# Kernel optimization log

Hardware: AMD Instinct MI355X
Metric: run time of the kernel (lower is better)

The kernel has to match this reference:

```python
import jax, jax.numpy as jnp
import numpy as np

N_NODES = 100000
N_EDGES = 1600000
N_ETYPES = 3
IN_FEATS = 128
HEADS = 4
OUT_FEATS = 16
EDGE_FEATS = 64
NEG_SLOPE = 0.2


def setup_inputs() -> dict:
    key = jax.random.key(0)
    ks = jax.random.split(key, 10)
    return {
        "x": jax.random.normal(ks[0], (N_NODES, IN_FEATS), jnp.float32),
        "W": jax.random.normal(ks[1], (IN_FEATS, HEADS * OUT_FEATS), jnp.float32) * 0.05,
        "W_e": jax.random.normal(ks[2], (EDGE_FEATS, HEADS * EDGE_FEATS), jnp.float32) * 0.05,
        "attn_l": jax.random.normal(ks[3], (HEADS, OUT_FEATS), jnp.float32) * 0.1,
        "attn_r": jax.random.normal(ks[4], (HEADS, OUT_FEATS), jnp.float32) * 0.1,
        "attn_e": jax.random.normal(ks[5], (HEADS, EDGE_FEATS), jnp.float32) * 0.1,
        "edge_emb": jax.random.normal(ks[6], (N_ETYPES, EDGE_FEATS), jnp.float32),
        "src": jax.random.randint(ks[7], (N_EDGES,), 0, N_NODES, jnp.int32),
        "dst": jax.random.randint(ks[8], (N_EDGES,), 0, N_NODES, jnp.int32),
        "etype": jax.random.randint(ks[9], (N_EDGES,), 0, N_ETYPES, jnp.int32),
    }


def reference(x, W, W_e, attn_l, attn_r, attn_e, edge_emb, src, dst, etype):
    N = x.shape[0]
    H, D = attn_l.shape
    # node projection: [N, H, D]
    feat = (x @ W).reshape(N, H, D)
    # per-node attention halves: [N, H]
    el = jnp.einsum("nhd,hd->nh", feat, attn_l)
    er = jnp.einsum("nhd,hd->nh", feat, attn_r)
    # per-etype edge term: [T, H]
    e_feat = (edge_emb @ W_e).reshape(edge_emb.shape[0], H, -1)
    ee = jnp.einsum("the,he->th", e_feat, attn_e)
    # per-edge pre-softmax score: [E, H]
    s = el[src] + er[dst] + ee[etype]
    s = jnp.where(s > 0, s, NEG_SLOPE * s)  # leaky_relu
    # edge softmax over incoming edges of each dst node (homogeneous graph)
    m = jax.ops.segment_max(s, dst, num_segments=N)
    e = jnp.exp(s - m[dst])
    z = jax.ops.segment_sum(e, dst, num_segments=N)
    a = e / z[dst]  # [E, H]
    # u_mul_e + sum aggregation: [N, H, D]
    msg = feat[src] * a[:, :, None]
    rst = jax.ops.segment_sum(msg, dst, num_segments=N)
    return rst, a
```

## Files before the change

### kernel.cpp

```cpp
#include <hip/hip_runtime.h>
#include <hip/hip_bf16.h>

#define N_NODES   100000
#define N_EDGES   1600000
#define N_ETYPES  3
#define IN_FEATS  128
#define HEADS     4
#define OUT_FEATS 16
#define EDGE_FEATS 64
#define HD        64
#define NEG_SLOPE 0.2f
#define MAXD_LDS  128

#define NBUCK     800
#define NPB       125
#define PBLK      400
#define EPB       4000
#define BCAP      2560

typedef short s16x8 __attribute__((ext_vector_type(8)));
typedef float f32x4 __attribute__((ext_vector_type(4)));

__device__ __forceinline__ short f2bs(float f) {
    __hip_bfloat16 h = __float2bfloat16(f);
    return *reinterpret_cast<short*>(&h);
}

__global__ __launch_bounds__(256) void wt_prep_kernel(
    const float* __restrict__ W, short* __restrict__ WTb)
{
    const int t = blockIdx.x * 256 + threadIdx.x;
    const int k = t >> 6, n = t & 63;
    WTb[n * IN_FEATS + k] = f2bs(W[t]);
}

#define XS_STRIDE 136
__global__ __launch_bounds__(256) void feat_el_er_kernel(
    const float* __restrict__ x,
    const short* __restrict__ WTb,
    const float* __restrict__ attn_l,
    const float* __restrict__ attn_r,
    __hip_bfloat16* __restrict__ featb,
    float* __restrict__ el,
    float* __restrict__ er)
{
    __shared__ short Xs[16 * XS_STRIDE];
    __shared__ short Ws[64 * XS_STRIDE];

    const int t = threadIdx.x;
    const int row0 = blockIdx.x * 16;
    {
        const int r = t >> 4, k0 = (t & 15) * 8;
        const float4* xg = (const float4*)(x + (size_t)(row0 + r) * IN_FEATS + k0);
        const float4 v0 = xg[0], v1 = xg[1];
        s16x8 p;
        p[0] = f2bs(v0.x); p[1] = f2bs(v0.y); p[2] = f2bs(v0.z); p[3] = f2bs(v0.w);
        p[4] = f2bs(v1.x); p[5] = f2bs(v1.y); p[6] = f2bs(v1.z); p[7] = f2bs(v1.w);
        *(s16x8*)&Xs[r * XS_STRIDE + k0] = p;
    }
    {
#pragma unroll
        for (int j = 0; j < 4; ++j) {
            const int u = t + 256 * j;
            const int r = u >> 4, c = (u & 15) * 8;
            *(s16x8*)&Ws[r * XS_STRIDE + c] = *(const s16x8*)(WTb + r * IN_FEATS + c);
        }
    }
    __syncthreads();

    const int w    = t >> 6;
    const int lane = t & 63;
    const int m    = lane & 15;
    const int q    = lane >> 4;

    f32x4 acc = {0.f, 0.f, 0.f, 0.f};
#pragma unroll
    for (int kb = 0; kb < 4; ++kb) {
        const s16x8 af = *(const s16x8*)&Xs[m * XS_STRIDE + kb * 32 + q * 8];
        const s16x8 bf = *(const s16x8*)&Ws[(w * 16 + m) * XS_STRIDE + kb * 32 + q * 8];
        acc = __builtin_amdgcn_mfma_f32_16x16x32_bf16(af, bf, acc, 0, 0, 0);
    }

    const float al = attn_l[w * OUT_FEATS + m];
    const float ar = attn_r[w * OUT_FEATS + m];
#pragma unroll
    for (int r = 0; r < 4; ++r) {
        const int row = row0 + q * 4 + r;
        featb[(size_t)row * HD + w * 16 + m] = __float2bfloat16(acc[r]);
        float cl = acc[r] * al;
        float cr = acc[r] * ar;
#pragma unroll
        for (int msk = 1; msk < 16; msk <<= 1) {
            cl += __shfl_xor(cl, msk, 64);
            cr += __shfl_xor(cr, msk, 64);
        }
        if (m == 0) {
            el[row * HEADS + w] = cl;
            er[row * HEADS + w] = cr;
        }
    }
}

__global__ __launch_bounds__(64) void ee_kernel(
    const float* __restrict__ edge_emb,
    const float* __restrict__ W_e,
    const float* __restrict__ attn_e,
    float* __restrict__ ee)
{
    const int b  = blockIdx.x;
    const int ty = b >> 2;
    const int h  = b & 3;
    const int e  = threadIdx.x;

    float ef = 0.f;
#pragma unroll
    for (int k = 0; k < EDGE_FEATS; ++k)
        ef += edge_emb[ty * EDGE_FEATS + k] *
              W_e[k * (HEADS * EDGE_FEATS) + h * EDGE_FEATS + e];
    float v = ef * attn_e[h * EDGE_FEATS + e];
#pragma unroll
    for (int m = 1; m < 64; m <<= 1) v += __shfl_xor(v, m, 64);
    if (e == 0) ee[ty * HEADS + h] = v;
}

__global__ __launch_bounds__(256) void bucket_hist_kernel(
    const int* __restrict__ dst, int* __restrict__ bhist)
{
    __shared__ int h[NBUCK];
    const int t = threadIdx.x, b = blockIdx.x;
    for (int j = t; j < NBUCK; j += 256) h[j] = 0;
    __syncthreads();
    const int e0 = b * EPB;
    for (int i = t; i < EPB; i += 256)
        atomicAdd(&h[dst[e0 + i] / NPB], 1);
    __syncthreads();
    for (int j = t; j < NBUCK; j += 256) bhist[b * NBUCK + j] = h[j];
}

__global__ __launch_bounds__(256) void bucket_scan1_kernel(
    int* __restrict__ bhist, int* __restrict__ btot)
{
    __shared__ int sh[PBLK];
    const int t = threadIdx.x, j = blockIdx.x;
    const int j0 = t, j1 = t + 256;
    int o0 = 0, o1 = 0;
    if (j0 < PBLK) { o0 = bhist[j0 * NBUCK + j]; sh[j0] = o0; }
    if (j1 < PBLK) { o1 = bhist[j1 * NBUCK + j]; sh[j1] = o1; }
    __syncthreads();
    for (int off = 1; off < PBLK; off <<= 1) {
        int v0 = (j0 >= off && j0 < PBLK) ? sh[j0 - off] : 0;
        int v1 = (j1 >= off && j1 < PBLK) ? sh[j1 - off] : 0;
        __syncthreads();
        if (j0 < PBLK) sh[j0] += v0;
        if (j1 < PBLK) sh[j1] += v1;
        __syncthreads();
    }
    if (j0 < PBLK) bhist[j0 * NBUCK + j] = sh[j0] - o0;
    if (j1 < PBLK) bhist[j1 * NBUCK + j] = sh[j1] - o1;
    if (t == 255) btot[j] = sh[PBLK - 1];
}

__global__ __launch_bounds__(1024) void bucket_scan2_kernel(
    const int* __restrict__ btot, int* __restrict__ bbase)
{
    __shared__ int sh[NBUCK];
    const int t = threadIdx.x;
    int o = 0;
    if (t < NBUCK) { o = btot[t]; sh[t] = o; }
    __syncthreads();
    for (int off = 1; off < NBUCK; off <<= 1) {
        int v = (t >= off && t < NBUCK) ? sh[t - off] : 0;
        __syncthreads();
        if (t < NBUCK) sh[t] += v;
        __syncthreads();
    }
    if (t < NBUCK) bbase[t] = sh[t] - o;
    if (t == NBUCK - 1) bbase[NBUCK] = sh[t];
}

__global__ __launch_bounds__(256) void bucket_scatter_kernel(
    const int* __restrict__ src, const int* __restrict__ dst,
    const int* __restrict__ etype,
    const int* __restrict__ bhist, const int* __restrict__ bbase,
    int2* __restrict__ sc_bucket)
{
    __shared__ int cnt[NBUCK];
    const int t = threadIdx.x, b = blockIdx.x;
    for (int j = t; j < NBUCK; j += 256)
        cnt[j] = bbase[j] + bhist[b * NBUCK + j];
    __syncthreads();
    const int e0 = b * EPB;
    for (int i = t; i < EPB; i += 256) {
        const int e  = e0 + i;
        const int dn = dst[e];
        const int bu = dn / NPB;
        const int ld = dn - bu * NPB;
        const int slot = atomicAdd(&cnt[bu], 1);
        sc_bucket[slot] = make_int2(src[e], e | (etype[e] << 21) | (ld << 23));
    }
}

__global__ __launch_bounds__(256) void bucket_csr_kernel(
    const int2* __restrict__ sc_bucket, const int* __restrict__ bbase,
    int* __restrict__ ptr, int2* __restrict__ sc_csr)
{
    __shared__ int2 sbuf[BCAP];
    __shared__ int sdeg[128];
    __shared__ int scur[128];
    const int t = threadIdx.x, b = blockIdx.x;
    const int lo = bbase[b];
    const int count = bbase[b + 1] - lo;
    const bool staged = (count <= BCAP);

    if (t < 128) sdeg[t] = 0;
    __syncthreads();
    if (staged) {
        for (int i = t; i < count; i += 256) {
            const int2 v = sc_bucket[lo + i];
            sbuf[i] = v;
            atomicAdd(&sdeg[(v.y >> 23) & 0x7F], 1);
        }
    } else {
        for (int i = t; i < count; i += 256)
            atomicAdd(&sdeg[(sc_bucket[lo + i].y >> 23) & 0x7F], 1);
    }
    __syncthreads();
    const int orig = (t < 128) ? sdeg[t] : 0;
    for (int off = 1; off < 128; off <<= 1) {
        const int v = (t < 128 && t >= off) ? sdeg[t - off] : 0;
        __syncthreads();
        if (t < 128) sdeg[t] += v;
        __syncthreads();
    }
    if (t < 128) {
        const int excl = sdeg[t] - orig;
        if (t < NPB) ptr[b * NPB + t] = lo + excl;
        scur[t] = lo + excl;
    }
    if (b == 0 && t == 0) ptr[N_NODES] = N_EDGES;
    __syncthreads();
    if (staged) {
        for (int i = t; i < count; i += 256) {
            const int2 v = sbuf[i];
            const int ld = (v.y >> 23) & 0x7F;
            const int slot = atomicAdd(&scur[ld], 1);
            sc_csr[slot] = make_int2(v.x, (v.y & 0x1FFFFF) | (((v.y >> 21) & 3) << 24));
        }
    } else {
        for (int i = t; i < count; i += 256) {
            const int2 v = sc_bucket[lo + i];
            const int ld = (v.y >> 23) & 0x7F;
            const int slot = atomicAdd(&scur[ld], 1);
            sc_csr[slot] = make_int2(v.x, (v.y & 0x1FFFFF) | (((v.y >> 21) & 3) << 24));
        }
    }
}

__global__ __launch_bounds__(256) void agg_kernel(
    const int2* __restrict__ sc_csr, const int* __restrict__ ptr,
    const float* __restrict__ el, const float* __restrict__ er,
    const float* __restrict__ ee, const __hip_bfloat16* __restrict__ featb,
    float* __restrict__ rst, float* __restrict__ a_out)
{
    __shared__ float w_lds[4][MAXD_LDS * HEADS];
    const int wid  = threadIdx.x >> 6;
    const int lane = threadIdx.x & 63;
    const int n    = blockIdx.x * 4 + wid;

    const int p0  = ptr[n];
    const int deg = ptr[n + 1] - p0;
    float* wl = w_lds[wid];
    const ushort* fb = (const ushort*)featb;

    if (deg <= MAXD_LDS) {
        const int half  = lane >> 5;
        const int cpair = lane & 31;
        const int hB    = cpair >> 3;
        const bool accL = (cpair & 7) == 0;
        const float er_n = er[n * HEADS + hB];
        const float g0 = ee[hB], g1 = ee[HEADS + hB], g2 = ee[2 * HEADS + hB];

        float zacc = 0.f, rx = 0.f, ry = 0.f;
        int i = 0;
        for (; i + 4 <= deg; i += 4) {
            const int2 sc0 = sc_csr[p0 + i + half];
            const int2 sc1 = sc_csr[p0 + i + 2 + half];
            const uint f0 = *(const uint*)(fb + ((size_t)sc0.x << 6) + (cpair << 1));
            const uint f1 = *(const uint*)(fb + ((size_t)sc1.x << 6) + (cpair << 1));
            const float el0 = el[sc0.x * HEADS + hB];
            const float el1 = el[sc1.x * HEADS + hB];
            const int ty0 = sc0.y >> 24, ty1 = sc1.y >> 24;
            float s0 = el0 + er_n + ((ty0 == 0) ? g0 : ((ty0 == 1) ? g1 : g2));
            float s1 = el1 + er_n + ((ty1 == 0) ? g0 : ((ty1 == 1) ? g1 : g2));
            s0 = s0 > 0.f ? s0 : NEG_SLOPE * s0;
            s1 = s1 > 0.f ? s1 : NEG_SLOPE * s1;
            const float w0 = __expf(s0), w1 = __expf(s1);
            if (accL) {
                zacc += w0 + w1;
                wl[(i + half) * HEADS + hB]     = w0;
                wl[(i + 2 + half) * HEADS + hB] = w1;
            }
            rx += __uint_as_float(f0 << 16) * w0 + __uint_as_float(f1 << 16) * w1;
            ry += __uint_as_float(f0 & 0xFFFF0000u) * w0 + __uint_as_float(f1 & 0xFFFF0000u) * w1;
        }
        if (i + 2 <= deg) {
            const int2 sc0 = sc_csr[p0 + i + half];
            const uint f0 = *(const uint*)(fb + ((size_t)sc0.x << 6) + (cpair << 1));
            const float el0 = el[sc0.x * HEADS + hB];
            const int ty0 = sc0.y >> 24;
            float s0 = el0 + er_n + ((ty0 == 0) ? g0 : ((ty0 == 1) ? g1 : g2));
            s0 = s0 > 0.f ? s0 : NEG_SLOPE * s0;
            const float w0 = __expf(s0);
            if (accL) {
                zacc += w0;
                wl[(i + half) * HEADS + hB] = w0;
            }
            rx += __uint_as_float(f0 << 16) * w0;
            ry += __uint_as_float(f0 & 0xFFFF0000u) * w0;
            i += 2;
        }
        if (i < deg) {
            if (half == 0) {
                const int2 sc0 = sc_csr[p0 + i];
                const uint f0 = *(const uint*)(fb + ((size_t)sc0.x << 6) + (cpair << 1));
                const float el0 = el[sc0.x * HEADS + hB];
                const int ty0 = sc0.y >> 24;
                float s0 = el0 + er_n + ((ty0 == 0) ? g0 : ((ty0 == 1) ? g1 : g2));
                s0 = s0 > 0.f ? s0 : NEG_SLOPE * s0;
                const float w0 = __expf(s0);
                if (accL) {
                    zacc += w0;
                    wl[i * HEADS + hB] = w0;
                }
                rx += __uint_as_float(f0 << 16) * w0;
                ry += __uint_as_float(f0 & 0xFFFF0000u) * w0;
            }
        }
        zacc += __shfl_xor(zacc, 32, 64);
        const float inv_z = (deg > 0) ? __frcp_rn(__shfl(zacc, hB << 3, 64)) : 0.f;

        rx += __shfl_xor(rx, 32, 64);
        ry += __shfl_xor(ry, 32, 64);
        if (half == 0) {
            float2 v = make_float2(rx * inv_z, ry * inv_z);
            *(float2*)(rst + (size_t)n * HD + (cpair << 1)) = v;
        }
        const int hA = lane & 3;
        const int eo = lane >> 2;
        const float inv_zA = (deg > 0) ? __frcp_rn(__shfl(zacc, hA << 3, 64)) : 0.f;
        for (int idx = eo; idx < deg; idx += 16) {
            const int ey = sc_csr[p0 + idx].y & 0xFFFFFF;
            a_out[(size_t)ey * HEADS + hA] = wl[idx * HEADS + hA] * inv_zA;
        }
    } else {
        const int hA = lane & 3;
        const int eo = lane >> 2;
        const float er_nA = er[n * HEADS + hA];
        const float a0 = ee[hA], a1 = ee[HEADS + hA], a2 = ee[2 * HEADS + hA];
        float zacc = 0.f;
        for (int base = 0; base < deg; base += 16) {
            const int idx = base + eo;
            if (idx < deg) {
                const int2 sc = sc_csr[p0 + idx];
                const int ty = sc.y >> 24;
                float s = el[sc.x * HEADS + hA] + er_nA + ((ty == 0) ? a0 : ((ty == 1) ? a1 : a2));
                s = s > 0.f ? s : NEG_SLOPE * s;
                zacc += __expf(s);
            }
        }
#pragma unroll
        for (int m = 4; m < 64; m <<= 1) zacc += __shfl_xor(zacc, m, 64);
        const int h = lane >> 4;
        const int d = lane & 15;
        const float inv_z = __frcp_rn(__shfl(zacc, h, 64));
        const float er_n = er[n * HEADS + h];
        const float g0 = ee[h], g1 = ee[HEADS + h], g2 = ee[2 * HEADS + h];
        float racc = 0.f;
        for (int i = 0; i < deg; ++i) {
            const int2 sc = sc_csr[p0 + i];
            const int ty = sc.y >> 24;
            float s = el[sc.x * HEADS + h] + er_n + ((ty == 0) ? g0 : ((ty == 1) ? g1 : g2));
            s = s > 0.f ? s : NEG_SLOPE * s;
            const float a = __expf(s) * inv_z;
            racc += __bfloat162float(featb[(size_t)sc.x * HD + lane]) * a;
            if (d == 0) a_out[(size_t)(sc.y & 0xFFFFFF) * HEADS + h] = a;
        }
        rst[(size_t)n * HD + lane] = racc;
    }
}

extern "C" void kernel_launch(void* const* d_in, const int* in_sizes, int n_in,
                              void* d_out, int out_size, void* d_ws, size_t ws_size,
                              hipStream_t stream)
{
    const float* x        = (const float*)d_in[0];
    const float* W        = (const float*)d_in[1];
    const float* W_e      = (const float*)d_in[2];
    const float* attn_l   = (const float*)d_in[3];
    const float* attn_r   = (const float*)d_in[4];
    const float* attn_e   = (const float*)d_in[5];
    const float* edge_emb = (const float*)d_in[6];
    const int* src   = (const int*)d_in[7];
    const int* dst   = (const int*)d_in[8];
    const int* etype = (const int*)d_in[9];

    float* out     = (float*)d_out;
    float* rst_out = out;
    float* a_out   = out + (size_t)N_NODES * HD;

    char* w = (char*)d_ws;
    __hip_bfloat16* featb = (__hip_bfloat16*)w; w += (size_t)N_NODES * HD * 2;
    float* el    = (float*)w;  w += (size_t)N_NODES * HEADS * 4;
    float* er    = (float*)w;  w += (size_t)N_NODES * HEADS * 4;
    float* ee    = (float*)w;  w += 64;
    int*   ptr   = (int*)w;    w += (size_t)(N_NODES + 4) * 4;
    int*   bhist = (int*)w;    w += (size_t)PBLK * NBUCK * 4;
    int*   btot  = (int*)w;    w += (size_t)NBUCK * 4;
    int*   bbase = (int*)w;    w += (size_t)(NBUCK + 4) * 4;
    short* WTb   = (short*)w;  w += (size_t)HD * IN_FEATS * 2;
    int2*  sc_bucket = (int2*)w; w += (size_t)N_EDGES * 8;
    int2*  sc_csr    = (int2*)w; w += (size_t)N_EDGES * 8;

    wt_prep_kernel<<<(IN_FEATS * HD) / 256, 256, 0, stream>>>(W, WTb);
    feat_el_er_kernel<<<N_NODES / 16, 256, 0, stream>>>(
        x, WTb, attn_l, attn_r, featb, el, er);
    ee_kernel<<<N_ETYPES * HEADS, 64, 0, stream>>>(edge_emb, W_e, attn_e, ee);

    bucket_hist_kernel<<<PBLK, 256, 0, stream>>>(dst, bhist);
    bucket_scan1_kernel<<<NBUCK, 256, 0, stream>>>(bhist, btot);
    bucket_scan2_kernel<<<1, 1024, 0, stream>>>(btot, bbase);
    bucket_scatter_kernel<<<PBLK, 256, 0, stream>>>(src, dst, etype, bhist, bbase, sc_bucket);
    bucket_csr_kernel<<<NBUCK, 256, 0, stream>>>(sc_bucket, bbase, ptr, sc_csr);

    agg_kernel<<<N_NODES / 4, 256, 0, stream>>>(
        sc_csr, ptr, el, er, ee, featb, rst_out, a_out);
}
```

Baseline: 288.4 us.

## Write attention outputs in edge order via separate kernel using stored inverse normalizers

The aggregation kernel no longer scatters per-edge attention to random edge IDs. It stores per-node inverse softmax sums, and a new edge-parallel kernel recomputes scores and writes a_out coalesced in edge order. The aggregation loop is also restructured into a two-phase form: it first computes weights and source IDs into LDS, then does a gather with 8-byte feature loads across 4 edge groups. The cost is recomputing exp per edge plus extra gathers of el, er and invz by src and dst, and the invz buffer aliases the sc_bucket scratch space.

```diff
diff --git a/kernel.cpp b/kernel.cpp
--- a/kernel.cpp
+++ b/kernel.cpp
@@ -260,9 +260,10 @@
     const int2* __restrict__ sc_csr, const int* __restrict__ ptr,
     const float* __restrict__ el, const float* __restrict__ er,
     const float* __restrict__ ee, const __hip_bfloat16* __restrict__ featb,
-    float* __restrict__ rst, float* __restrict__ a_out)
+    float* __restrict__ rst, float* __restrict__ invz)
 {
     __shared__ float w_lds[4][MAXD_LDS * HEADS];
+    __shared__ int   s_lds[4][MAXD_LDS];
     const int wid  = threadIdx.x >> 6;
     const int lane = threadIdx.x & 63;
     const int n    = blockIdx.x * 4 + wid;
@@ -270,87 +271,76 @@
     const int p0  = ptr[n];
     const int deg = ptr[n + 1] - p0;
     float* wl = w_lds[wid];
+    int*   sl = s_lds[wid];
     const ushort* fb = (const ushort*)featb;
 
     if (deg <= MAXD_LDS) {
-        const int half  = lane >> 5;
-        const int cpair = lane & 31;
-        const int hB    = cpair >> 3;
-        const bool accL = (cpair & 7) == 0;
-        const float er_n = er[n * HEADS + hB];
-        const float g0 = ee[hB], g1 = ee[HEADS + hB], g2 = ee[2 * HEADS + hB];
-
-        float zacc = 0.f, rx = 0.f, ry = 0.f;
+        const int eo = lane >> 2;
+        const int hA = lane & 3;
+        const float er_n = er[n * HEADS + hA];
+        const float g0 = ee[hA], g1 = ee[HEADS + hA], g2 = ee[2 * HEADS + hA];
+
+        float zacc = 0.f;
+        for (int i0 = 0; i0 < deg; i0 += 16) {
+            const int idx = i0 + eo;
+            float w = 0.f;
+            if (idx < deg) {
+                const int2 sc = sc_csr[p0 + idx];
+                const int ty = sc.y >> 24;
+                float s = el[sc.x * HEADS + hA] + er_n +
+                          ((ty == 0) ? g0 : ((ty == 1) ? g1 : g2));
+                s = s > 0.f ? s : NEG_SLOPE * s;
+                w = __expf(s);
+                wl[idx * HEADS + hA] = w;
+                if (hA == 0) sl[idx] = sc.x;
+            }
+            zacc += w;
+        }
+        zacc += __shfl_xor(zacc, 4, 64);
+        zacc += __shfl_xor(zacc, 8, 64);
+        zacc += __shfl_xor(zacc, 16, 64);
+        zacc += __shfl_xor(zacc, 32, 64);
+        if (lane < 4)
+            invz[n * HEADS + lane] = (deg > 0) ? __frcp_rn(zacc) : 0.f;
+
+        const int q  = lane >> 4;
+        const int c  = lane & 15;
+        const int hB = c >> 2;
+        const float inv_z = (deg > 0) ? __frcp_rn(__shfl(zacc, hB, 64)) : 0.f;
+
+        float a0 = 0.f, a1 = 0.f, a2 = 0.f, a3 = 0.f;
         int i = 0;
-        for (; i + 4 <= deg; i += 4) {
-            const int2 sc0 = sc_csr[p0 + i + half];
-            const int2 sc1 = sc_csr[p0 + i + 2 + half];
-            const uint f0 = *(const uint*)(fb + ((size_t)sc0.x << 6) + (cpair << 1));
-            const uint f1 = *(const uint*)(fb + ((size_t)sc1.x << 6) + (cpair << 1));
-            const float el0 = el[sc0.x * HEADS + hB];
-            const float el1 = el[sc1.x * HEADS + hB];
-            const int ty0 = sc0.y >> 24, ty1 = sc1.y >> 24;
-            float s0 = el0 + er_n + ((ty0 == 0) ? g0 : ((ty0 == 1) ? g1 : g2));
-            float s1 = el1 + er_n + ((ty1 == 0) ? g0 : ((ty1 == 1) ? g1 : g2));
-            s0 = s0 > 0.f ? s0 : NEG_SLOPE * s0;
-            s1 = s1 > 0.f ? s1 : NEG_SLOPE * s1;
-            const float w0 = __expf(s0), w1 = __expf(s1);
-            if (accL) {
-                zacc += w0 + w1;
-                wl[(i + half) * HEADS + hB]     = w0;
-                wl[(i + 2 + half) * HEADS + hB] = w1;
+        for (; i + 8 <= deg; i += 8) {
+            const int idxA = i + q, idxB = i + 4 + q;
+            const int sA = sl[idxA], sB = sl[idxB];
+            const float wA = wl[idxA * HEADS + hB];
+            const float wB = wl[idxB * HEADS + hB];
+            const uint2 fA = *(const uint2*)(fb + ((size_t)sA << 6) + (c << 2));
+            const uint2 fB = *(const uint2*)(fb + ((size_t)sB << 6) + (c << 2));
+            a0 += __uint_as_float(fA.x << 16) * wA + __uint_as_float(fB.x << 16) * wB;
+            a1 += __uint_as_float(fA.x & 0xFFFF0000u) * wA + __uint_as_float(fB.x & 0xFFFF0000u) * wB;
+            a2 += __uint_as_float(fA.y << 16) * wA + __uint_as_float(fB.y << 16) * wB;
+            a3 += __uint_as_float(fA.y & 0xFFFF0000u) * wA + __uint_as_float(fB.y & 0xFFFF0000u) * wB;
+        }
+        for (; i < deg; i += 4) {
+            const int idx = i + q;
+            if (idx < deg) {
+                const int sA = sl[idx];
+                const float wA = wl[idx * HEADS + hB];
+                const uint2 fA = *(const uint2*)(fb + ((size_t)sA << 6) + (c << 2));
+                a0 += __uint_as_float(fA.x << 16) * wA;
+                a1 += __uint_as_float(fA.x & 0xFFFF0000u) * wA;
+                a2 += __uint_as_float(fA.y << 16) * wA;
+                a3 += __uint_as_float(fA.y & 0xFFFF0000u) * wA;
             }
-            rx += __uint_as_float(f0 << 16) * w0 + __uint_as_float(f1 << 16) * w1;
-            ry += __uint_as_float(f0 & 0xFFFF0000u) * w0 + __uint_as_float(f1 & 0xFFFF0000u) * w1;
-        }
-        if (i + 2 <= deg) {
-            const int2 sc0 = sc_csr[p0 + i + half];
-            const uint f0 = *(const uint*)(fb + ((size_t)sc0.x << 6) + (cpair << 1));
-            const float el0 = el[sc0.x * HEADS + hB];
-            const int ty0 = sc0.y >> 24;
-            float s0 = el0 + er_n + ((ty0 == 0) ? g0 : ((ty0 == 1) ? g1 : g2));
-            s0 = s0 > 0.f ? s0 : NEG_SLOPE * s0;
-            const float w0 = __expf(s0);
-            if (accL) {
-                zacc += w0;
-                wl[(i + half) * HEADS + hB] = w0;
-            }
-            rx += __uint_as_float(f0 << 16) * w0;
-            ry += __uint_as_float(f0 & 0xFFFF0000u) * w0;
-            i += 2;
-        }
-        if (i < deg) {
-            if (half == 0) {
-                const int2 sc0 = sc_csr[p0 + i];
-                const uint f0 = *(const uint*)(fb + ((size_t)sc0.x << 6) + (cpair << 1));
-                const float el0 = el[sc0.x * HEADS + hB];
-                const int ty0 = sc0.y >> 24;
-                float s0 = el0 + er_n + ((ty0 == 0) ? g0 : ((ty0 == 1) ? g1 : g2));
-                s0 = s0 > 0.f ? s0 : NEG_SLOPE * s0;
-                const float w0 = __expf(s0);
-                if (accL) {
-                    zacc += w0;
-                    wl[i * HEADS + hB] = w0;
-                }
-                rx += __uint_as_float(f0 << 16) * w0;
-                ry += __uint_as_float(f0 & 0xFFFF0000u) * w0;
-            }
-        }
-        zacc += __shfl_xor(zacc, 32, 64);
-        const float inv_z = (deg > 0) ? __frcp_rn(__shfl(zacc, hB << 3, 64)) : 0.f;
-
-        rx += __shfl_xor(rx, 32, 64);
-        ry += __shfl_xor(ry, 32, 64);
-        if (half == 0) {
-            float2 v = make_float2(rx * inv_z, ry * inv_z);
-            *(float2*)(rst + (size_t)n * HD + (cpair << 1)) = v;
-        }
-        const int hA = lane & 3;
-        const int eo = lane >> 2;
-        const float inv_zA = (deg > 0) ? __frcp_rn(__shfl(zacc, hA << 3, 64)) : 0.f;
-        for (int idx = eo; idx < deg; idx += 16) {
-            const int ey = sc_csr[p0 + idx].y & 0xFFFFFF;
-            a_out[(size_t)ey * HEADS + hA] = wl[idx * HEADS + hA] * inv_zA;
+        }
+        a0 += __shfl_xor(a0, 16, 64); a0 += __shfl_xor(a0, 32, 64);
+        a1 += __shfl_xor(a1, 16, 64); a1 += __shfl_xor(a1, 32, 64);
+        a2 += __shfl_xor(a2, 16, 64); a2 += __shfl_xor(a2, 32, 64);
+        a3 += __shfl_xor(a3, 16, 64); a3 += __shfl_xor(a3, 32, 64);
+        if (q == 0) {
+            f32x4 v = {a0 * inv_z, a1 * inv_z, a2 * inv_z, a3 * inv_z};
+            *(f32x4*)(rst + (size_t)n * HD + (c << 2)) = v;
         }
     } else {
         const int hA = lane & 3;
@@ -370,8 +360,8 @@
         }
 #pragma unroll
         for (int m = 4; m < 64; m <<= 1) zacc += __shfl_xor(zacc, m, 64);
+        if (lane < 4) invz[n * HEADS + lane] = __frcp_rn(zacc);
         const int h = lane >> 4;
-        const int d = lane & 15;
         const float inv_z = __frcp_rn(__shfl(zacc, h, 64));
         const float er_n = er[n * HEADS + h];
         const float g0 = ee[h], g1 = ee[HEADS + h], g2 = ee[2 * HEADS + h];
@@ -383,10 +373,33 @@
             s = s > 0.f ? s : NEG_SLOPE * s;
             const float a = __expf(s) * inv_z;
             racc += __bfloat162float(featb[(size_t)sc.x * HD + lane]) * a;
-            if (d == 0) a_out[(size_t)(sc.y & 0xFFFFFF) * HEADS + h] = a;
         }
         rst[(size_t)n * HD + lane] = racc;
     }
+}
+
+__global__ __launch_bounds__(256) void attn_out_kernel(
+    const int* __restrict__ src, const int* __restrict__ dst,
+    const int* __restrict__ etype,
+    const float* __restrict__ el, const float* __restrict__ er,
+    const float* __restrict__ ee, const float* __restrict__ invz,
+    float* __restrict__ a_out)
+{
+    const int e = blockIdx.x * 256 + threadIdx.x;
+    const int sN = src[e];
+    const int dN = dst[e];
+    const int ty = etype[e];
+    const float4 l4 = *(const float4*)(el + (size_t)sN * HEADS);
+    const float4 r4 = *(const float4*)(er + (size_t)dN * HEADS);
+    const float4 g4 = *(const float4*)(ee + (size_t)ty * HEADS);
+    const float4 iz = *(const float4*)(invz + (size_t)dN * HEADS);
+    float4 a;
+    float s;
+    s = l4.x + r4.x + g4.x; s = s > 0.f ? s : NEG_SLOPE * s; a.x = __expf(s) * iz.x;
+    s = l4.y + r4.y + g4.y; s = s > 0.f ? s : NEG_SLOPE * s; a.y = __expf(s) * iz.y;
+    s = l4.z + r4.z + g4.z; s = s > 0.f ? s : NEG_SLOPE * s; a.z = __expf(s) * iz.z;
+    s = l4.w + r4.w + g4.w; s = s > 0.f ? s : NEG_SLOPE * s; a.w = __expf(s) * iz.w;
+    *(float4*)(a_out + (size_t)e * HEADS) = a;
 }
 
 extern "C" void kernel_launch(void* const* d_in, const int* in_sizes, int n_in,
@@ -421,6 +434,8 @@
     int2*  sc_bucket = (int2*)w; w += (size_t)N_EDGES * 8;
     int2*  sc_csr    = (int2*)w; w += (size_t)N_EDGES * 8;
 
+    float* invz = (float*)sc_bucket;
+
     wt_prep_kernel<<<(IN_FEATS * HD) / 256, 256, 0, stream>>>(W, WTb);
     feat_el_er_kernel<<<N_NODES / 16, 256, 0, stream>>>(
         x, WTb, attn_l, attn_r, featb, el, er);
@@ -433,5 +448,7 @@
     bucket_csr_kernel<<<NBUCK, 256, 0, stream>>>(sc_bucket, bbase, ptr, sc_csr);
 
     agg_kernel<<<N_NODES / 4, 256, 0, stream>>>(
-        sc_csr, ptr, el, er, ee, featb, rst_out, a_out);
-}
+        sc_csr, ptr, el, er, ee, featb, rst_out, invz);
+    attn_out_kernel<<<N_EDGES / 256, 256, 0, stream>>>(
+        src, dst, etype, el, er, ee, invz, a_out);
+}
```

New measurement: 289.5 us. Within noise of the previous version (+0.4%).
